# Performance work log

Measured on AMD Instinct MI355X. Metric: run time of the kernel, lower is better.

The kernel has to match this reference:

```python
import jax, jax.numpy as jnp
import numpy as np

D_C, D_K, D_T = 1024, 1024, 1024
N_KB = 65536
BATCH = 4096
ALPHA_C, ALPHA_K, ALPHA_T = 1.0, 0.5, 0.25


def setup_inputs() -> dict:
    key = jax.random.key(0)
    k1, k2, k3 = jax.random.split(key, 3)
    C = jax.random.normal(k1, (BATCH, D_C), dtype=jnp.float32)
    K = jax.random.normal(k2, (BATCH, D_K), dtype=jnp.float32)
    tie_kb = jax.random.normal(k3, (N_KB, D_T), dtype=jnp.float32)
    # Frozen Q: zero-initialized then identity on the top-left min(D_C, D_T) block.
    Q_weight = jnp.zeros((D_T, D_C), dtype=jnp.float32)
    d = min(D_C, D_T)
    Q_weight = Q_weight.at[:d, :d].set(jnp.eye(d, dtype=jnp.float32))
    return {
        "C": C,
        "K": K,
        "tie_kb": tie_kb,
        "Q_weight": Q_weight,
        "temperature": 1.0,
        "top_k": 32,
    }


def _retrieve_tie_batched(q, kb, top_k, temperature):
    """Batched version of the per-row retrieve_tie: cdist -> top-k nearest ->
    softmax(-dist/temperature) weighted sum of KB rows.
    q: [n, D_T], kb: [N_kb, D_T] -> [n, D_T]
    """
    q_sq = jnp.sum(q * q, axis=-1, keepdims=True)            # [n, 1]
    kb_sq = jnp.sum(kb * kb, axis=-1)                        # [N_kb]
    # Squared Euclidean distances via GEMM (same math as torch.cdist p=2)
    d2 = jnp.maximum(q_sq + kb_sq[None, :] - 2.0 * (q @ kb.T), 0.0)  # [n, N_kb]
    dist = jnp.sqrt(d2)
    neg_top, idx = jax.lax.top_k(-dist, top_k)               # top_k smallest dists
    w = jax.nn.softmax(neg_top / temperature, axis=-1)       # [n, top_k]
    sel = kb[idx]                                            # [n, top_k, D_T]
    return jnp.einsum('nk,nkd->nd', w, sel)


def reference(C, K, tie_kb, Q_weight, temperature, top_k):
    q = C @ Q_weight.T                                       # [n, D_T]
    T = _retrieve_tie_batched(q, tie_kb, top_k, temperature)  # [n, D_T]
    fused = jnp.concatenate([ALPHA_C * C, ALPHA_K * K, ALPHA_T * T], axis=1)
    return jax.nn.silu(fused)
```

## Files before the change

kernel.cpp:

```cpp
#include <hip/hip_runtime.h>
#include <stdint.h>

#define D_DIM   1024
#define NKB     65536
#define BATCH   4096
#define TOPK    32
#define NCHUNKS 16
#define CHUNK   4096
#define MT      128
#define NT      128
#define BKK     64
#define RB      16
#define RB_P    17

typedef float  floatx4 __attribute__((ext_vector_type(4)));
typedef __bf16 bf16x8  __attribute__((ext_vector_type(8)));

__device__ __forceinline__ uint16_t f2bf(float f) {
  union { float f; uint32_t i; } v; v.f = f;
  return (uint16_t)((v.i + 0x7fffu + ((v.i >> 16) & 1u)) >> 16);
}
__device__ __forceinline__ float silu_f(float x) { return x / (1.f + __expf(-x)); }

__device__ __forceinline__ void gl_lds16(const uint16_t* g, uint16_t* l) {
  __builtin_amdgcn_global_load_lds((const __attribute__((address_space(1))) void*)g,
                                   (__attribute__((address_space(3))) void*)l,
                                   16, 0, 0);
}

__global__ void convert_norms_kernel(const float* __restrict__ KB,
                                     const float* __restrict__ C,
                                     uint16_t* __restrict__ KBb,
                                     uint16_t* __restrict__ Cb,
                                     float* __restrict__ kbsq,
                                     float* __restrict__ qsq) {
  int wid  = (blockIdx.x * blockDim.x + threadIdx.x) >> 6;
  int lane = threadIdx.x & 63;
  if (wid >= NKB + BATCH) return;
  const float* src; uint16_t* dst;
  if (wid < NKB) { src = KB + (size_t)wid * D_DIM; dst = KBb + (size_t)wid * D_DIM; }
  else { src = C + (size_t)(wid - NKB) * D_DIM; dst = Cb + (size_t)(wid - NKB) * D_DIM; }

  const float4* p = (const float4*)src;
  uint4* q = (uint4*)dst;
  float s = 0.f;
  float4 f[4];
#pragma unroll
  for (int h = 0; h < 4; ++h) f[h] = p[lane * 4 + h];
  uint32_t ob[8];
#pragma unroll
  for (int h = 0; h < 4; ++h) {
    float vv[4] = {f[h].x, f[h].y, f[h].z, f[h].w};
#pragma unroll
    for (int e = 0; e < 4; ++e) s += vv[e] * vv[e];
    ob[h * 2]     = (uint32_t)f2bf(vv[0]) | ((uint32_t)f2bf(vv[1]) << 16);
    ob[h * 2 + 1] = (uint32_t)f2bf(vv[2]) | ((uint32_t)f2bf(vv[3]) << 16);
  }
  q[lane * 2]     = (uint4){ob[0], ob[1], ob[2], ob[3]};
  q[lane * 2 + 1] = (uint4){ob[4], ob[5], ob[6], ob[7]};
#pragma unroll
  for (int off = 32; off > 0; off >>= 1) s += __shfl_xor(s, off);
  if (lane == 0) { if (wid < NKB) kbsq[wid] = s; else qsq[wid - NKB] = s; }
}

__launch_bounds__(256, 2)
__global__ void dist_topk_kernel(const uint16_t* __restrict__ Cb,
                                 const uint16_t* __restrict__ KBb,
                                 const float* __restrict__ kbsq,
                                 const float* __restrict__ qsq,
                                 float* __restrict__ cand_d,
                                 int*   __restrict__ cand_i) {
  __shared__ __align__(16) uint16_t As[MT * BKK];
  __shared__ __align__(16) uint16_t Bs[NT * BKK];
  __shared__ float    rbd[MT * RB_P];
  __shared__ uint16_t rbi[MT * RB_P];
  __shared__ int      rbcnt[MT];
  __shared__ float    thr[MT];
  __shared__ float    qsq_l[MT];
  __shared__ int      s_any;

  const int t = threadIdx.x;
  const int w = t >> 6, lane = t & 63;
  const int lm = lane & 15, lq = lane >> 4;
  const int wr = w >> 1, wc = w & 1;
  const int row0 = blockIdx.x * MT;
  const int col0 = blockIdx.y * CHUNK;

  float tv[TOPK]; int ti[TOPK];
#pragma unroll
  for (int k = 0; k < TOPK; ++k) { tv[k] = __builtin_inff(); ti[k] = 0; }

  if (t < MT) { thr[t] = __builtin_inff(); rbcnt[t] = 0; qsq_l[t] = qsq[row0 + t]; }
  if (t == 0) s_any = 0;
  __syncthreads();

  for (int ct = 0; ct < CHUNK / NT; ++ct) {
    const int cb = col0 + ct * NT;
    floatx4 acc[4][4];
#pragma unroll
    for (int i = 0; i < 4; ++i)
#pragma unroll
      for (int j = 0; j < 4; ++j) acc[i][j] = (floatx4){0.f, 0.f, 0.f, 0.f};

    for (int k0 = 0; k0 < D_DIM; k0 += BKK) {
      __syncthreads();
#pragma unroll
      for (int is = 0; is < 4; ++is) {
        int c = is * 256 + t;
        int row = c >> 3, kp = c & 7;
        int kps = kp ^ (row & 7);
        gl_lds16(Cb + (size_t)(row0 + row) * D_DIM + k0 + kps * 8,
                 &As[(is * 256 + (w << 6)) * 8]);
      }
#pragma unroll
      for (int is = 0; is < 4; ++is) {
        int c = is * 256 + t;
        int row = c >> 3, kp = c & 7;
        int kps = kp ^ (row & 7);
        gl_lds16(KBb + (size_t)(cb + row) * D_DIM + k0 + kps * 8,
                 &Bs[(is * 256 + (w << 6)) * 8]);
      }
      __syncthreads();
#pragma unroll
      for (int kk = 0; kk < 2; ++kk) {
        bf16x8 af[4], bf[4];
#pragma unroll
        for (int i = 0; i < 4; ++i) {
          int r = (wr << 6) + (i << 4) + lm;
          int p = (kk * 4 + lq) ^ (r & 7);
          af[i] = *(const bf16x8*)&As[r * BKK + p * 8];
        }
#pragma unroll
        for (int j = 0; j < 4; ++j) {
          int r = (wc << 6) + (j << 4) + lm;
          int p = (kk * 4 + lq) ^ (r & 7);
          bf[j] = *(const bf16x8*)&Bs[r * BKK + p * 8];
        }
#pragma unroll
        for (int i = 0; i < 4; ++i)
#pragma unroll
          for (int j = 0; j < 4; ++j)
            acc[i][j] = __builtin_amdgcn_mfma_f32_16x16x32_bf16(af[i], bf[j], acc[i][j], 0, 0, 0);
      }
    }

    float kbc[4];
#pragma unroll
    for (int j = 0; j < 4; ++j) kbc[j] = kbsq[cb + (wc << 6) + (j << 4) + lm];

    uint64_t pend = 0;
#pragma unroll
    for (int i = 0; i < 4; ++i) {
#pragma unroll
      for (int rg = 0; rg < 4; ++rg) {
        int rl = (wr << 6) + (i << 4) + (lq << 2) + rg;
        float qv = qsq_l[rl];
        float th = thr[rl];
#pragma unroll
        for (int j = 0; j < 4; ++j) {
          float d2 = fmaf(-2.f, acc[i][j][rg], qv + kbc[j]);
          if (d2 < th) {
            int slot = atomicAdd(&rbcnt[rl], 1);
            if (slot < RB) {
              rbd[rl * RB_P + slot] = d2;
              rbi[rl * RB_P + slot] = (uint16_t)(cb + (wc << 6) + (j << 4) + lm);
            } else pend |= 1ull << ((i << 4) | (rg << 2) | j);
          }
        }
      }
    }
    __syncthreads();

    while (true) {
      if (t < MT) {
        int n = rbcnt[t]; if (n > RB) n = RB;
        for (int e = 0; e < n; ++e) {
          float d = rbd[t * RB_P + e];
          int  ix = rbi[t * RB_P + e];
          if (d < tv[TOPK - 1]) {
#pragma unroll
            for (int p = TOPK - 1; p >= 1; --p) {
              bool lt_prev = d < tv[p - 1];
              bool lt_here = d < tv[p];
              float nv = lt_prev ? tv[p - 1] : (lt_here ? d : tv[p]);
              int   ni = lt_prev ? ti[p - 1] : (lt_here ? ix : ti[p]);
              tv[p] = nv; ti[p] = ni;
            }
            if (d < tv[0]) { tv[0] = d; ti[0] = ix; }
          }
        }
        rbcnt[t] = 0;
        thr[t] = tv[TOPK - 1];
      }
      __syncthreads();
      if (pend) s_any = 1;
      __syncthreads();
      if (!s_any) break;
      uint64_t np = 0;
#pragma unroll
      for (int i = 0; i < 4; ++i) {
#pragma unroll
        for (int rg = 0; rg < 4; ++rg) {
          int rl = (wr << 6) + (i << 4) + (lq << 2) + rg;
#pragma unroll
          for (int j = 0; j < 4; ++j) {
            const int v = (i << 4) | (rg << 2) | j;
            if (pend & (1ull << v)) {
              float d2 = fmaf(-2.f, acc[i][j][rg], qsq_l[rl] + kbc[j]);
              if (d2 < thr[rl]) {
                int slot = atomicAdd(&rbcnt[rl], 1);
                if (slot < RB) {
                  rbd[rl * RB_P + slot] = d2;
                  rbi[rl * RB_P + slot] = (uint16_t)(cb + (wc << 6) + (j << 4) + lm);
                } else np |= 1ull << v;
              }
            }
          }
        }
      }
      pend = np;
      __syncthreads();
      if (t == 0) s_any = 0;
      __syncthreads();
    }
  }

  if (t < MT) {
    size_t base = ((size_t)(row0 + t) * NCHUNKS + blockIdx.y) * TOPK;
#pragma unroll
    for (int k = 0; k < TOPK; ++k) {
      cand_d[base + k] = tv[k];
      cand_i[base + k] = ti[k];
    }
  }
}

__global__ void merge_kernel(const float* __restrict__ Cm,
                             const float* __restrict__ Km,
                             const float* __restrict__ KB,
                             const float* __restrict__ cand_d,
                             const int*   __restrict__ cand_i,
                             float* __restrict__ out) {
  __shared__ float sel_d[4][TOPK];
  __shared__ int   sel_i[4][TOPK];
  __shared__ float wgt[4][TOPK];
  int w = threadIdx.x >> 6, lane = threadIdx.x & 63;
  int R = blockIdx.x * 4 + w;

  float v[8]; int ix[8];
#pragma unroll
  for (int s = 0; s < 8; ++s) {
    v[s]  = cand_d[(size_t)R * (NCHUNKS * TOPK) + s * 64 + lane];
    ix[s] = cand_i[(size_t)R * (NCHUNKS * TOPK) + s * 64 + lane];
  }
  for (int k = 0; k < TOPK; ++k) {
    float bm = v[0]; int bs = 0;
#pragma unroll
    for (int s = 1; s < 8; ++s) if (v[s] < bm) { bm = v[s]; bs = s; }
    float m = bm; int ml = lane;
#pragma unroll
    for (int off = 32; off > 0; off >>= 1) {
      float om = __shfl_xor(m, off);
      int   ol = __shfl_xor(ml, off);
      if (om < m || (om == m && ol < ml)) { m = om; ml = ol; }
    }
    if (lane == ml) { sel_d[w][k] = bm; sel_i[w][k] = ix[bs]; v[bs] = __builtin_inff(); }
  }
  float dmin = sqrtf(fmaxf(sel_d[w][0], 0.f));
  float e = 0.f;
  if (lane < TOPK) e = __expf(dmin - sqrtf(fmaxf(sel_d[w][lane], 0.f)));
  float sum = e;
#pragma unroll
  for (int off = 32; off > 0; off >>= 1) sum += __shfl_xor(sum, off);
  if (lane < TOPK) wgt[w][lane] = e / sum;

  float accT[16];
#pragma unroll
  for (int s = 0; s < 16; ++s) accT[s] = 0.f;
  int d0 = lane * 16;
  for (int k = 0; k < TOPK; ++k) {
    int idx = sel_i[w][k] & 0xFFFF;
    float wk = wgt[w][k];
    const float4* kp = (const float4*)(KB + (size_t)idx * D_DIM + d0);
#pragma unroll
    for (int h = 0; h < 4; ++h) {
      float4 q = kp[h];
      accT[h * 4 + 0] = fmaf(wk, q.x, accT[h * 4 + 0]);
      accT[h * 4 + 1] = fmaf(wk, q.y, accT[h * 4 + 1]);
      accT[h * 4 + 2] = fmaf(wk, q.z, accT[h * 4 + 2]);
      accT[h * 4 + 3] = fmaf(wk, q.w, accT[h * 4 + 3]);
    }
  }

  size_t ob = (size_t)R * 3072;
  const float4* cp  = (const float4*)(Cm + (size_t)R * D_DIM + d0);
  const float4* kp2 = (const float4*)(Km + (size_t)R * D_DIM + d0);
#pragma unroll
  for (int h = 0; h < 4; ++h) {
    float4 c = cp[h], kq = kp2[h], o;
    o.x = silu_f(c.x); o.y = silu_f(c.y); o.z = silu_f(c.z); o.w = silu_f(c.w);
    ((float4*)&out[ob + d0])[h] = o;
    o.x = silu_f(0.5f * kq.x); o.y = silu_f(0.5f * kq.y);
    o.z = silu_f(0.5f * kq.z); o.w = silu_f(0.5f * kq.w);
    ((float4*)&out[ob + 1024 + d0])[h] = o;
    o.x = silu_f(0.25f * accT[h * 4 + 0]); o.y = silu_f(0.25f * accT[h * 4 + 1]);
    o.z = silu_f(0.25f * accT[h * 4 + 2]); o.w = silu_f(0.25f * accT[h * 4 + 3]);
    ((float4*)&out[ob + 2048 + d0])[h] = o;
  }
}

extern "C" void kernel_launch(void* const* d_in, const int* in_sizes, int n_in,
                              void* d_out, int out_size, void* d_ws, size_t ws_size,
                              hipStream_t stream) {
  (void)in_sizes; (void)n_in; (void)out_size; (void)ws_size;
  const float* Cm = (const float*)d_in[0];
  const float* Km = (const float*)d_in[1];
  const float* KB = (const float*)d_in[2];
  uint8_t* ws = (uint8_t*)d_ws;
  uint16_t* KBb  = (uint16_t*)ws;
  uint16_t* Cb   = (uint16_t*)(ws + 134217728);
  float*    kbsq = (float*)(ws + 134217728 + 8388608);
  float*    qsq  = (float*)(ws + 134217728 + 8388608 + 262144);
  float*    cand_d = (float*)(ws + 142884864);
  int*      cand_i = (int*)(ws + 142884864 + 8388608);
  float*    out  = (float*)d_out;

  convert_norms_kernel<<<dim3((NKB + BATCH) / 4), 256, 0, stream>>>(KB, Cm, KBb, Cb, kbsq, qsq);
  dist_topk_kernel<<<dim3(BATCH / MT, NCHUNKS), 256, 0, stream>>>(Cb, KBb, kbsq, qsq, cand_d, cand_i);
  merge_kernel<<<dim3(BATCH / 4), 256, 0, stream>>>(Cm, Km, KB, cand_d, cand_i, out);
}
```

Before: 1.646 ms.

## Defer candidate ring-buffer drain to overlap with next tile's global loads

Instead of draining the per-row candidate buffers right after each column tile's GEMM, with extra barriers, the drain is postponed into the next tile's first k-step, after the async global-to-LDS loads are issued. The overflow retry loop only runs when some thread reported pending entries, which removes barriers on the common path. The thresholds used for filtering the next tile are now one tile stale, so more candidates may pass into the buffers and overflow more often.

```diff
diff --git a/kernel.cpp b/kernel.cpp
--- a/kernel.cpp
+++ b/kernel.cpp
@@ -90,9 +90,32 @@
 #pragma unroll
   for (int k = 0; k < TOPK; ++k) { tv[k] = __builtin_inff(); ti[k] = 0; }
 
+  auto drain_rb = [&](int tt) {
+    int n = rbcnt[tt]; if (n > RB) n = RB;
+    for (int e = 0; e < n; ++e) {
+      float d = rbd[tt * RB_P + e];
+      int  iv = rbi[tt * RB_P + e];
+      if (d < tv[TOPK - 1]) {
+#pragma unroll
+        for (int p = TOPK - 1; p >= 1; --p) {
+          bool lt_prev = d < tv[p - 1];
+          bool lt_here = d < tv[p];
+          float nv = lt_prev ? tv[p - 1] : (lt_here ? d : tv[p]);
+          int   ni = lt_prev ? ti[p - 1] : (lt_here ? iv : ti[p]);
+          tv[p] = nv; ti[p] = ni;
+        }
+        if (d < tv[0]) { tv[0] = d; ti[0] = iv; }
+      }
+    }
+    rbcnt[tt] = 0;
+    thr[tt] = tv[TOPK - 1];
+  };
+
   if (t < MT) { thr[t] = __builtin_inff(); rbcnt[t] = 0; qsq_l[t] = qsq[row0 + t]; }
   if (t == 0) s_any = 0;
   __syncthreads();
+
+  bool pending = false;
 
   for (int ct = 0; ct < CHUNK / NT; ++ct) {
     const int cb = col0 + ct * NT;
@@ -119,6 +142,10 @@
         int kps = kp ^ (row & 7);
         gl_lds16(KBb + (size_t)(cb + row) * D_DIM + k0 + kps * 8,
                  &Bs[(is * 256 + (w << 6)) * 8]);
+      }
+      if (k0 == 0 && pending) {
+        if (t < MT) drain_rb(t);
+        pending = false;
       }
       __syncthreads();
 #pragma unroll
@@ -169,60 +196,48 @@
         }
       }
     }
+    if (pend) s_any = 1;
     __syncthreads();
 
-    while (true) {
-      if (t < MT) {
-        int n = rbcnt[t]; if (n > RB) n = RB;
-        for (int e = 0; e < n; ++e) {
-          float d = rbd[t * RB_P + e];
-          int  ix = rbi[t * RB_P + e];
-          if (d < tv[TOPK - 1]) {
-#pragma unroll
-            for (int p = TOPK - 1; p >= 1; --p) {
-              bool lt_prev = d < tv[p - 1];
-              bool lt_here = d < tv[p];
-              float nv = lt_prev ? tv[p - 1] : (lt_here ? d : tv[p]);
-              int   ni = lt_prev ? ti[p - 1] : (lt_here ? ix : ti[p]);
-              tv[p] = nv; ti[p] = ni;
-            }
-            if (d < tv[0]) { tv[0] = d; ti[0] = ix; }
-          }
-        }
-        rbcnt[t] = 0;
-        thr[t] = tv[TOPK - 1];
-      }
-      __syncthreads();
-      if (pend) s_any = 1;
-      __syncthreads();
-      if (!s_any) break;
-      uint64_t np = 0;
-#pragma unroll
-      for (int i = 0; i < 4; ++i) {
-#pragma unroll
-        for (int rg = 0; rg < 4; ++rg) {
-          int rl = (wr << 6) + (i << 4) + (lq << 2) + rg;
-#pragma unroll
-          for (int j = 0; j < 4; ++j) {
-            const int v = (i << 4) | (rg << 2) | j;
-            if (pend & (1ull << v)) {
-              float d2 = fmaf(-2.f, acc[i][j][rg], qsq_l[rl] + kbc[j]);
-              if (d2 < thr[rl]) {
-                int slot = atomicAdd(&rbcnt[rl], 1);
-                if (slot < RB) {
-                  rbd[rl * RB_P + slot] = d2;
-                  rbi[rl * RB_P + slot] = (uint16_t)(cb + (wc << 6) + (j << 4) + lm);
-                } else np |= 1ull << v;
+    if (s_any) {
+      while (true) {
+        if (t < MT) drain_rb(t);
+        if (t == 0) s_any = 0;
+        __syncthreads();
+        uint64_t np = 0;
+#pragma unroll
+        for (int i = 0; i < 4; ++i) {
+#pragma unroll
+          for (int rg = 0; rg < 4; ++rg) {
+            int rl = (wr << 6) + (i << 4) + (lq << 2) + rg;
+#pragma unroll
+            for (int j = 0; j < 4; ++j) {
+              const int v = (i << 4) | (rg << 2) | j;
+              if (pend & (1ull << v)) {
+                float d2 = fmaf(-2.f, acc[i][j][rg], qsq_l[rl] + kbc[j]);
+                if (d2 < thr[rl]) {
+                  int slot = atomicAdd(&rbcnt[rl], 1);
+                  if (slot < RB) {
+                    rbd[rl * RB_P + slot] = d2;
+                    rbi[rl * RB_P + slot] = (uint16_t)(cb + (wc << 6) + (j << 4) + lm);
+                  } else np |= 1ull << v;
+                }
               }
             }
           }
         }
-      }
-      pend = np;
-      __syncthreads();
-      if (t == 0) s_any = 0;
-      __syncthreads();
-    }
+        pend = np;
+        if (pend) s_any = 1;
+        __syncthreads();
+        if (!s_any) break;
+      }
+    } else {
+      pending = true;
+    }
+  }
+
+  if (pending) {
+    if (t < MT) drain_rb(t);
   }
 
   if (t < MT) {
```

Result: no change. 1.660 ms (+0.8%).
